# Kernel tuning notes

Hardware: AMD Instinct MI355X
Metric: run time of the kernel (lower is better)

The kernel has to match this reference:

```python
import jax, jax.numpy as jnp
import numpy as np

P, F_IN, HG, C, T, E, HOUT = 4096, 64, 64, 64, 32, 65536, 12
LEAKY_SLOPE = 0.2
LN_EPS = 1e-5


def setup_inputs() -> dict:
    key = jax.random.key(0)
    ks = jax.random.split(key, 14)
    g = lambda k, shape, scale: (jax.random.normal(k, shape, jnp.float32) * scale)
    return {
        "X": jax.random.normal(ks[0], (1, P, F_IN, T), jnp.float32),
        "edge_index": jax.random.randint(ks[1], (T, 2, E), 0, P, jnp.int32),
        # GATv2 params (single head)
        "Wl": g(ks[2], (F_IN, HG), 0.1),
        "Wr": g(ks[3], (F_IN, HG), 0.1),
        "att": g(ks[4], (HG,), 0.1),
        "gat_b": g(ks[5], (HG,), 0.02),
        # 1x1 time conv (HG -> C) and 1x1 residual conv (F_IN -> C)
        "W_time": g(ks[6], (C, HG), 0.1),
        "b_time": g(ks[7], (C,), 0.02),
        "W_res": g(ks[8], (C, F_IN), 0.1),
        "b_res": g(ks[9], (C,), 0.02),
        # LayerNorm over channel dim C
        "ln_g": jnp.ones((C,), jnp.float32),
        "ln_b": jnp.zeros((C,), jnp.float32),
        # final conv: Conv2d(in=T, out=HOUT, kernel=(1, C)) -> weight (HOUT, T, C)
        "W_final": g(ks[10], (HOUT, T, C), 0.05),
        "b_final": g(ks[11], (HOUT,), 0.02),
    }


def reference(X, edge_index, Wl, Wr, att, gat_b, W_time, b_time, W_res, b_res,
              ln_g, ln_b, W_final, b_final):
    Pn = X.shape[1]

    def gat_t(x, edges):
        # x: (P, F_IN), edges: (2, E) with edges[0]=src j, edges[1]=dst i
        src, dst = edges[0], edges[1]
        hl = x @ Wl                      # (P, HG) messages
        hr = x @ Wr                      # (P, HG) query side
        e = jax.nn.leaky_relu(hl[src] + hr[dst], LEAKY_SLOPE) @ att  # (E,)
        emax = jax.ops.segment_max(e, dst, num_segments=Pn)
        ex = jnp.exp(e - emax[dst])
        den = jax.ops.segment_sum(ex, dst, num_segments=Pn)
        alpha = ex / den[dst]            # softmax over in-edges of each dst
        return jax.ops.segment_sum(alpha[:, None] * hl[src], dst,
                                   num_segments=Pn) + gat_b  # (P, HG)

    xs = jnp.moveaxis(X[0], -1, 0)                     # (T, P, F_IN)
    X_hat = jax.nn.relu(jax.vmap(gat_t)(xs, edge_index))  # (T, P, HG)

    th = jnp.einsum('tph,ch->tpc', X_hat, W_time) + b_time  # time conv 1x1
    rs = jnp.einsum('tpf,cf->tpc', xs, W_res) + b_res       # residual conv 1x1
    y = jax.nn.relu(th + rs)                                 # (T, P, C)

    mu = jnp.mean(y, axis=-1, keepdims=True)
    var = jnp.var(y, axis=-1, keepdims=True)
    yn = (y - mu) * jax.lax.rsqrt(var + LN_EPS) * ln_g + ln_b  # (T, P, C)

    # final conv: in-channels = T, kernel (1, C) -> contract over t and c
    out = jnp.einsum('tpc,otc->po', yn, W_final) + b_final     # (P, HOUT)
    return out[None]                                           # (1, P, HOUT)
```

## Files before the change

### kernel.cpp

```cpp
#include <hip/hip_runtime.h>
#include <math.h>

#define NP 4096
#define F_IN 64
#define HG 64
#define NC 64
#define NT 32
#define NE 65536
#define HOUT 12
#define LEAKY 0.2f
#define LN_EPS 1e-5f
#define CAPC 32

template <int CTRL>
__device__ __forceinline__ float dppadd(float v, float x) {
    int r = __builtin_amdgcn_update_dpp(0, __builtin_bit_cast(int, x), CTRL, 0xF, 0xF, false);
    return v + __builtin_bit_cast(float, r);
}
__device__ __forceinline__ float rowsum16(float v) {
    v = dppadd<0x128>(v, v);
    v = dppadd<0x124>(v, v);
    v = dppadd<0x122>(v, v);
    v = dppadd<0x121>(v, v);
    return v;
}
__device__ __forceinline__ float laneXorSum(float v) {
    v += __shfl_xor(v, 16, 64);
    v += __shfl_xor(v, 32, 64);
    return v;
}

#define FMA4(Acomp, B, r)                                                     \
    acc[r][0] += (Acomp) * (B).x; acc[r][1] += (Acomp) * (B).y;               \
    acc[r][2] += (Acomp) * (B).z; acc[r][3] += (Acomp) * (B).w;

__global__ __launch_bounds__(256) void k_front(const float* __restrict__ X,
        const float* __restrict__ Wl, const float* __restrict__ Wr,
        const float* __restrict__ W_res, const float* __restrict__ b_res,
        const float* __restrict__ W_time, const float* __restrict__ bf,
        const int* __restrict__ EI,
        float* __restrict__ hl, float* __restrict__ hr, float* __restrict__ rs,
        float* __restrict__ wtT, float* __restrict__ out,
        int* __restrict__ cnt, unsigned short* __restrict__ scap) {
    __shared__ float smem[8960];
    int b = blockIdx.x;
    int tid = threadIdx.x;
    if (b < 512) {
        unsigned short (*buck)[CAPC] = (unsigned short (*)[CAPC])smem;
        int* cnts = (int*)(smem + 8192);
        int t = (b & 7) + 8 * ((b >> 3) & 3);
        int rem = b >> 5;
        int c = rem & 1, r = rem >> 1;
        cnts[tid] = 0; cnts[tid + 256] = 0;
        __syncthreads();
        const int4* srcA = (const int4*)(EI + (size_t)t * 2 * NE) + c * (NE / 8);
        const int4* dstA = (const int4*)(EI + (size_t)t * 2 * NE + NE) + c * (NE / 8);
        for (int i = tid; i < NE / 8; i += 256) {
            int4 s = srcA[i];
            int4 d = dstA[i];
            if ((d.x >> 9) == r) { int lo = d.x & 511; int sl = atomicAdd(&cnts[lo], 1); if (sl < CAPC) buck[lo][sl] = (unsigned short)s.x; }
            if ((d.y >> 9) == r) { int lo = d.y & 511; int sl = atomicAdd(&cnts[lo], 1); if (sl < CAPC) buck[lo][sl] = (unsigned short)s.y; }
            if ((d.z >> 9) == r) { int lo = d.z & 511; int sl = atomicAdd(&cnts[lo], 1); if (sl < CAPC) buck[lo][sl] = (unsigned short)s.z; }
            if ((d.w >> 9) == r) { int lo = d.w & 511; int sl = atomicAdd(&cnts[lo], 1); if (sl < CAPC) buck[lo][sl] = (unsigned short)s.w; }
        }
        __syncthreads();
        int obase = ((t * 2 + c) << 12) + (r << 9);
        cnt[obase + tid] = cnts[tid];
        cnt[obase + tid + 256] = cnts[tid + 256];
        unsigned int* dstw = (unsigned int*)(scap + (size_t)obase * CAPC);
        const unsigned int* srcw = (const unsigned int*)buck;
        for (int i = tid; i < 512 * CAPC / 2; i += 256)
            dstw[i] = srcw[i];
    } else if (b < 2560) {
        float (*xs)[F_IN][36] = (float (*)[F_IN][36])smem;
        float (*bk)[68] = (float (*)[68])(smem + 4608);
        int p0 = (b - 512) * 2;
        const float4* Xp = (const float4*)(X + (size_t)p0 * F_IN * NT);
        for (int i4 = tid; i4 < 1024; i4 += 256) {
            int pp = i4 >> 9, f = (i4 >> 3) & 63, t0 = (i4 & 7) * 4;
            *(float4*)&xs[pp][f][t0] = Xp[i4];
        }
        int ng = tid & 15, pp = (tid >> 4) & 1, tg = tid >> 5;
        int n0 = ng * 4, t0 = tg * 4;
        {
            const float4* B4 = (const float4*)Wl;
            for (int i4 = tid; i4 < 1024; i4 += 256)
                *(float4*)&bk[i4 >> 4][(i4 & 15) * 4] = B4[i4];
            __syncthreads();
            float acc[4][4];
#pragma unroll
            for (int i = 0; i < 4; ++i)
#pragma unroll
                for (int j2 = 0; j2 < 4; ++j2) acc[i][j2] = 0.f;
#pragma unroll 8
            for (int f = 0; f < F_IN; ++f) {
                float4 B = *(const float4*)&bk[f][n0];
                float4 A = *(const float4*)&xs[pp][f][t0];
                FMA4(A.x, B, 0) FMA4(A.y, B, 1) FMA4(A.z, B, 2) FMA4(A.w, B, 3)
            }
#pragma unroll
            for (int i = 0; i < 4; ++i) {
                float4 v;
                v.x = acc[i][0]; v.y = acc[i][1]; v.z = acc[i][2]; v.w = acc[i][3];
                *(float4*)&hl[((size_t)(t0 + i) * NP + p0 + pp) * HG + n0] = v;
            }
            __syncthreads();
        }
        {
            const float4* B4 = (const float4*)Wr;
            for (int i4 = tid; i4 < 1024; i4 += 256)
                *(float4*)&bk[i4 >> 4][(i4 & 15) * 4] = B4[i4];
            __syncthreads();
            float acc[4][4];
#pragma unroll
            for (int i = 0; i < 4; ++i)
#pragma unroll
                for (int j2 = 0; j2 < 4; ++j2) acc[i][j2] = 0.f;
#pragma unroll 8
            for (int f = 0; f < F_IN; ++f) {
                float4 B = *(const float4*)&bk[f][n0];
                float4 A = *(const float4*)&xs[pp][f][t0];
                FMA4(A.x, B, 0) FMA4(A.y, B, 1) FMA4(A.z, B, 2) FMA4(A.w, B, 3)
            }
#pragma unroll
            for (int i = 0; i < 4; ++i) {
                float4 v;
                v.x = acc[i][0]; v.y = acc[i][1]; v.z = acc[i][2]; v.w = acc[i][3];
                *(float4*)&hr[((size_t)(t0 + i) * NP + p0 + pp) * HG + n0] = v;
            }
            __syncthreads();
        }
        {
            for (int i = tid; i < F_IN * NC; i += 256) {
                int c = i >> 6, f = i & 63;
                bk[f][c] = W_res[i];
            }
            __syncthreads();
            float4 br4 = *(const float4*)&b_res[n0];
            float acc[4][4];
#pragma unroll
            for (int i = 0; i < 4; ++i) {
                acc[i][0] = br4.x; acc[i][1] = br4.y; acc[i][2] = br4.z; acc[i][3] = br4.w;
            }
#pragma unroll 8
            for (int f = 0; f < F_IN; ++f) {
                float4 B = *(const float4*)&bk[f][n0];
                float4 A = *(const float4*)&xs[pp][f][t0];
                FMA4(A.x, B, 0) FMA4(A.y, B, 1) FMA4(A.z, B, 2) FMA4(A.w, B, 3)
            }
#pragma unroll
            for (int i = 0; i < 4; ++i) {
                float4 v;
                v.x = acc[i][0]; v.y = acc[i][1]; v.z = acc[i][2]; v.w = acc[i][3];
                *(float4*)&rs[((size_t)(t0 + i) * NP + p0 + pp) * NC + n0] = v;
            }
        }
    } else if (b < 2576) {
        int i = (b - 2560) * 256 + tid;
        wtT[i] = W_time[(i & 63) * 64 + (i >> 6)];
    } else {
        int i = (b - 2576) * 256 + tid;
        out[i] = bf[i % HOUT];
    }
}

__global__ __launch_bounds__(256) void k_gat(const float* __restrict__ hl,
        float* __restrict__ hr,
        const int* __restrict__ cnt, const unsigned short* __restrict__ scap,
        const float* __restrict__ att, const float* __restrict__ gat_b) {
    __shared__ int sidx[4][64];
    int b = blockIdx.x;
    int k = b >> 3;
    int t = (b & 7) + 8 * (k >> 10);
    int ws = threadIdx.x >> 6;
    int i = (k & 1023) * 4 + ws;
    int lane = threadIdx.x & 63;
    int row = lane >> 4;
    int c0 = (lane & 15) * 4;
    size_t nbase = ((size_t)t * NP + i) * HG;
    const float* hlt = hl + (size_t)t * NP * HG;
    float4 r4 = *(const float4*)&hr[nbase + c0];
    float4 at4 = *(const float4*)&att[c0];
    int d0 = cnt[((t * 2 + 0) << 12) + i]; d0 = (d0 < CAPC) ? d0 : CAPC;
    int d1 = cnt[((t * 2 + 1) << 12) + i]; d1 = (d1 < CAPC) ? d1 : CAPC;
    int deg = d0 + d1;
    deg = (deg < 64) ? deg : 64;
    const unsigned short* s0 = scap + ((size_t)(((t * 2 + 0) << 12) + i)) * CAPC;
    const unsigned short* s1 = scap + ((size_t)(((t * 2 + 1) << 12) + i)) * CAPC;
    int li = (lane < deg) ? lane : 0;
    int f1 = (li >= d0);
    int idx = f1 ? (li - d0) : li;
    sidx[ws][lane] = (int)(f1 ? s1 : s0)[idx];
    float l = 0.f;
    float4 acc = {0.f, 0.f, 0.f, 0.f};
    int nfull = deg & ~7;
    int j = 0;
    for (; j < nfull; j += 8) {
        int src0 = sidx[ws][j + row];
        int src1 = sidx[ws][j + 4 + row];
        float4 h0 = *(const float4*)&hlt[((size_t)src0 << 6) + c0];
        float4 h1 = *(const float4*)&hlt[((size_t)src1 << 6) + c0];
        float4 z0, z1;
        z0.x = h0.x + r4.x; z0.y = h0.y + r4.y; z0.z = h0.z + r4.z; z0.w = h0.w + r4.w;
        z1.x = h1.x + r4.x; z1.y = h1.y + r4.y; z1.z = h1.z + r4.z; z1.w = h1.w + r4.w;
        z0.x = fmaxf(z0.x, LEAKY * z0.x); z0.y = fmaxf(z0.y, LEAKY * z0.y);
        z0.z = fmaxf(z0.z, LEAKY * z0.z); z0.w = fmaxf(z0.w, LEAKY * z0.w);
        z1.x = fmaxf(z1.x, LEAKY * z1.x); z1.y = fmaxf(z1.y, LEAKY * z1.y);
        z1.z = fmaxf(z1.z, LEAKY * z1.z); z1.w = fmaxf(z1.w, LEAKY * z1.w);
        float e0 = rowsum16(z0.x * at4.x + z0.y * at4.y + z0.z * at4.z + z0.w * at4.w);
        float e1 = rowsum16(z1.x * at4.x + z1.y * at4.y + z1.z * at4.z + z1.w * at4.w);
        float w0 = __expf(e0);
        float w1 = __expf(e1);
        l += w0 + w1;
        acc.x += w0 * h0.x + w1 * h1.x;
        acc.y += w0 * h0.y + w1 * h1.y;
        acc.z += w0 * h0.z + w1 * h1.z;
        acc.w += w0 * h0.w + w1 * h1.w;
    }
    for (; j < deg; j += 4) {
        int jj = j + row;
        int src = sidx[ws][(jj < deg) ? jj : 0];
        float4 ha = *(const float4*)&hlt[((size_t)src << 6) + c0];
        float4 za;
        za.x = ha.x + r4.x; za.y = ha.y + r4.y; za.z = ha.z + r4.z; za.w = ha.w + r4.w;
        za.x = fmaxf(za.x, LEAKY * za.x);
        za.y = fmaxf(za.y, LEAKY * za.y);
        za.z = fmaxf(za.z, LEAKY * za.z);
        za.w = fmaxf(za.w, LEAKY * za.w);
        float ep = za.x * at4.x + za.y * at4.y + za.z * at4.z + za.w * at4.w;
        float e = rowsum16(ep);
        float w = __expf(e);
        w = (jj < deg) ? w : 0.f;
        l += w;
        acc.x += w * ha.x; acc.y += w * ha.y; acc.z += w * ha.z; acc.w += w * ha.w;
    }
    float lt = laneXorSum(l);
    acc.x = laneXorSum(acc.x);
    acc.y = laneXorSum(acc.y);
    acc.z = laneXorSum(acc.z);
    acc.w = laneXorSum(acc.w);
    if (row == 0) {
        float inv = (deg > 0) ? (1.0f / lt) : 0.f;
        float4 gb = *(const float4*)&gat_b[c0];
        float4 o;
        o.x = fmaxf(acc.x * inv + gb.x, 0.f);
        o.y = fmaxf(acc.y * inv + gb.y, 0.f);
        o.z = fmaxf(acc.z * inv + gb.z, 0.f);
        o.w = fmaxf(acc.w * inv + gb.w, 0.f);
        *(float4*)&hr[nbase + c0] = o;
    }
}

__global__ __launch_bounds__(256) void k_pf(const float* __restrict__ Xhat,
        const float* __restrict__ wtT, const float* __restrict__ b_time,
        const float* __restrict__ rs, const float* __restrict__ ln_g,
        const float* __restrict__ ln_b, const float* __restrict__ Wf,
        float* __restrict__ out) {
    __shared__ float in_t[64][68];
    __shared__ float bk[64][68];
    int bx = blockIdx.x;
    int tc = bx & 15;
    int p0 = (bx >> 4) * 64;
    int tid = threadIdx.x;
    const float4* wsrc = (const float4*)wtT;
    for (int i4 = tid; i4 < 1024; i4 += 256) {
        int h = i4 >> 4, c4 = (i4 & 15) * 4;
        *(float4*)&bk[h][c4] = wsrc[i4];
    }
    int cg = tid & 15, pg = tid >> 4;
    int c0 = cg * 4, pl = pg * 4;
    float4 bt4 = *(const float4*)&b_time[c0];
    float4 lg = *(const float4*)&ln_g[c0];
    float4 lb = *(const float4*)&ln_b[c0];
    float ot[4][HOUT];
#pragma unroll
    for (int i = 0; i < 4; ++i)
#pragma unroll
        for (int o = 0; o < HOUT; ++o) ot[i][o] = 0.f;
    for (int ti = 0; ti < 2; ++ti) {
        int t = tc + ti * 16;
        __syncthreads();
        const float4* src = (const float4*)(Xhat + ((size_t)t * NP + p0) * HG);
        for (int i4 = tid; i4 < 1024; i4 += 256) {
            int pp = i4 >> 4, c4 = (i4 & 15) * 4;
            *(float4*)&in_t[pp][c4] = src[i4];
        }
        __syncthreads();
        float acc[4][4];
#pragma unroll
        for (int i = 0; i < 4; ++i) {
            acc[i][0] = bt4.x; acc[i][1] = bt4.y; acc[i][2] = bt4.z; acc[i][3] = bt4.w;
        }
#pragma unroll
        for (int k4 = 0; k4 < 16; ++k4) {
            float4 A0 = *(const float4*)&in_t[pl + 0][k4 * 4];
            float4 A1 = *(const float4*)&in_t[pl + 1][k4 * 4];
            float4 A2 = *(const float4*)&in_t[pl + 2][k4 * 4];
            float4 A3 = *(const float4*)&in_t[pl + 3][k4 * 4];
            float4 B0 = *(const float4*)&bk[k4 * 4 + 0][c0];
            FMA4(A0.x, B0, 0) FMA4(A1.x, B0, 1) FMA4(A2.x, B0, 2) FMA4(A3.x, B0, 3)
            float4 B1 = *(const float4*)&bk[k4 * 4 + 1][c0];
            FMA4(A0.y, B1, 0) FMA4(A1.y, B1, 1) FMA4(A2.y, B1, 2) FMA4(A3.y, B1, 3)
            float4 B2 = *(const float4*)&bk[k4 * 4 + 2][c0];
            FMA4(A0.z, B2, 0) FMA4(A1.z, B2, 1) FMA4(A2.z, B2, 2) FMA4(A3.z, B2, 3)
            float4 B3 = *(const float4*)&bk[k4 * 4 + 3][c0];
            FMA4(A0.w, B3, 0) FMA4(A1.w, B3, 1) FMA4(A2.w, B3, 2) FMA4(A3.w, B3, 3)
        }
        float4 ynv[4];
#pragma unroll
        for (int i = 0; i < 4; ++i) {
            size_t prow = (size_t)t * NP + p0 + pl + i;
            float4 r4 = *(const float4*)&rs[prow * NC + c0];
            float y0 = fmaxf(acc[i][0] + r4.x, 0.f), y1 = fmaxf(acc[i][1] + r4.y, 0.f);
            float y2 = fmaxf(acc[i][2] + r4.z, 0.f), y3 = fmaxf(acc[i][3] + r4.w, 0.f);
            float s = rowsum16(y0 + y1 + y2 + y3);
            float ss = rowsum16(y0 * y0 + y1 * y1 + y2 * y2 + y3 * y3);
            float mu = s * (1.f / 64.f);
            float var = ss * (1.f / 64.f) - mu * mu;
            float rsd = rsqrtf(var + LN_EPS);
            ynv[i].x = (y0 - mu) * rsd * lg.x + lb.x;
            ynv[i].y = (y1 - mu) * rsd * lg.y + lb.y;
            ynv[i].z = (y2 - mu) * rsd * lg.z + lb.z;
            ynv[i].w = (y3 - mu) * rsd * lg.w + lb.w;
        }
#pragma unroll
        for (int o = 0; o < HOUT; ++o) {
            float4 w4 = *(const float4*)&Wf[(size_t)o * NT * NC + t * NC + c0];
#pragma unroll
            for (int i = 0; i < 4; ++i)
                ot[i][o] += ynv[i].x * w4.x + ynv[i].y * w4.y
                          + ynv[i].z * w4.z + ynv[i].w * w4.w;
        }
    }
#pragma unroll
    for (int i = 0; i < 4; ++i)
#pragma unroll
        for (int o = 0; o < HOUT; ++o) ot[i][o] = rowsum16(ot[i][o]);
    if (cg == 0) {
#pragma unroll
        for (int i = 0; i < 4; ++i) {
            int p = p0 + pl + i;
#pragma unroll
            for (int o = 0; o < HOUT; ++o)
                atomicAdd(&out[p * HOUT + o], ot[i][o]);
        }
    }
}

extern "C" void kernel_launch(void* const* d_in, const int* in_sizes, int n_in,
                              void* d_out, int out_size, void* d_ws, size_t ws_size,
                              hipStream_t stream) {
    const float* X      = (const float*)d_in[0];
    const int*   EI     = (const int*)d_in[1];
    const float* Wl     = (const float*)d_in[2];
    const float* Wr     = (const float*)d_in[3];
    const float* att    = (const float*)d_in[4];
    const float* gat_b  = (const float*)d_in[5];
    const float* W_time = (const float*)d_in[6];
    const float* b_time = (const float*)d_in[7];
    const float* W_res  = (const float*)d_in[8];
    const float* b_res  = (const float*)d_in[9];
    const float* ln_g   = (const float*)d_in[10];
    const float* ln_b   = (const float*)d_in[11];
    const float* Wf     = (const float*)d_in[12];
    const float* bf     = (const float*)d_in[13];
    float* out = (float*)d_out;

    char* ws = (char*)d_ws;
    const size_t MB = 1024 * 1024;
    float* hl   = (float*)(ws);
    float* hr   = (float*)(ws + 32 * MB);
    float* rs   = (float*)(ws + 64 * MB);
    float* wtT  = (float*)(ws + 96 * MB);
    int*   cnt  = (int*)  (ws + 97 * MB);
    unsigned short* scap = (unsigned short*)(ws + 98 * MB);

    k_front<<<2768, 256, 0, stream>>>(X, Wl, Wr, W_res, b_res, W_time, bf, EI,
                                      hl, hr, rs, wtT, out, cnt, scap);
    k_gat  <<<(NT * NP) / 4, 256, 0, stream>>>(hl, hr, cnt, scap, att, gat_b);
    k_pf   <<<1024, 256, 0, stream>>>(hr, wtT, b_time, rs, ln_g, ln_b, Wf, out);
}
```

Baseline: 285.3 us.

## Fuse time conv, LayerNorm and final conv into GAT kernel with deterministic reduce

The GAT aggregation kernel now also performs the 1x1 time conv, residual add, LayerNorm and the per-timestep slice of the final conv. Each wave processes 8 nodes in a loop and keeps the W_time slice in registers. Per-timestep partial outputs go to a workspace buffer, and a small new kernel sums them over T and adds the bias, replacing the atomicAdd path and the out-initialisation blocks. This removes the X_hat write/read round trip and the separate k_pf GEMM. In exchange it adds register pressure (wreg[16]), serial per-node work per wave, and a third launch.

```diff
diff --git a/kernel.cpp b/kernel.cpp
--- a/kernel.cpp
+++ b/kernel.cpp
@@ -37,10 +37,10 @@
 __global__ __launch_bounds__(256) void k_front(const float* __restrict__ X,
         const float* __restrict__ Wl, const float* __restrict__ Wr,
         const float* __restrict__ W_res, const float* __restrict__ b_res,
-        const float* __restrict__ W_time, const float* __restrict__ bf,
+        const float* __restrict__ W_time,
         const int* __restrict__ EI,
         float* __restrict__ hl, float* __restrict__ hr, float* __restrict__ rs,
-        float* __restrict__ wtT, float* __restrict__ out,
+        float* __restrict__ wtT,
         int* __restrict__ cnt, unsigned short* __restrict__ scap) {
     __shared__ float smem[8960];
     int b = blockIdx.x;
@@ -155,196 +155,154 @@
                 *(float4*)&rs[((size_t)(t0 + i) * NP + p0 + pp) * NC + n0] = v;
             }
         }
-    } else if (b < 2576) {
+    } else {
         int i = (b - 2560) * 256 + tid;
         wtT[i] = W_time[(i & 63) * 64 + (i >> 6)];
-    } else {
-        int i = (b - 2576) * 256 + tid;
-        out[i] = bf[i % HOUT];
     }
 }
 
 __global__ __launch_bounds__(256) void k_gat(const float* __restrict__ hl,
-        float* __restrict__ hr,
+        const float* __restrict__ hr, const float* __restrict__ rs,
         const int* __restrict__ cnt, const unsigned short* __restrict__ scap,
-        const float* __restrict__ att, const float* __restrict__ gat_b) {
+        const float* __restrict__ att, const float* __restrict__ gat_b,
+        const float* __restrict__ wtT, const float* __restrict__ b_time,
+        const float* __restrict__ ln_g, const float* __restrict__ ln_b,
+        const float* __restrict__ Wf, float* __restrict__ pout) {
     __shared__ int sidx[4][64];
+    __shared__ float xbuf[4][64];
     int b = blockIdx.x;
-    int k = b >> 3;
-    int t = (b & 7) + 8 * (k >> 10);
+    int t = (b & 7) + 8 * (b >> 10);
+    int pc = (b >> 3) & 127;
     int ws = threadIdx.x >> 6;
-    int i = (k & 1023) * 4 + ws;
     int lane = threadIdx.x & 63;
     int row = lane >> 4;
-    int c0 = (lane & 15) * 4;
-    size_t nbase = ((size_t)t * NP + i) * HG;
+    int cg = lane & 15;
+    int c0 = cg * 4;
     const float* hlt = hl + (size_t)t * NP * HG;
-    float4 r4 = *(const float4*)&hr[nbase + c0];
     float4 at4 = *(const float4*)&att[c0];
-    int d0 = cnt[((t * 2 + 0) << 12) + i]; d0 = (d0 < CAPC) ? d0 : CAPC;
-    int d1 = cnt[((t * 2 + 1) << 12) + i]; d1 = (d1 < CAPC) ? d1 : CAPC;
-    int deg = d0 + d1;
-    deg = (deg < 64) ? deg : 64;
-    const unsigned short* s0 = scap + ((size_t)(((t * 2 + 0) << 12) + i)) * CAPC;
-    const unsigned short* s1 = scap + ((size_t)(((t * 2 + 1) << 12) + i)) * CAPC;
-    int li = (lane < deg) ? lane : 0;
-    int f1 = (li >= d0);
-    int idx = f1 ? (li - d0) : li;
-    sidx[ws][lane] = (int)(f1 ? s1 : s0)[idx];
-    float l = 0.f;
-    float4 acc = {0.f, 0.f, 0.f, 0.f};
-    int nfull = deg & ~7;
-    int j = 0;
-    for (; j < nfull; j += 8) {
-        int src0 = sidx[ws][j + row];
-        int src1 = sidx[ws][j + 4 + row];
-        float4 h0 = *(const float4*)&hlt[((size_t)src0 << 6) + c0];
-        float4 h1 = *(const float4*)&hlt[((size_t)src1 << 6) + c0];
-        float4 z0, z1;
-        z0.x = h0.x + r4.x; z0.y = h0.y + r4.y; z0.z = h0.z + r4.z; z0.w = h0.w + r4.w;
-        z1.x = h1.x + r4.x; z1.y = h1.y + r4.y; z1.z = h1.z + r4.z; z1.w = h1.w + r4.w;
-        z0.x = fmaxf(z0.x, LEAKY * z0.x); z0.y = fmaxf(z0.y, LEAKY * z0.y);
-        z0.z = fmaxf(z0.z, LEAKY * z0.z); z0.w = fmaxf(z0.w, LEAKY * z0.w);
-        z1.x = fmaxf(z1.x, LEAKY * z1.x); z1.y = fmaxf(z1.y, LEAKY * z1.y);
-        z1.z = fmaxf(z1.z, LEAKY * z1.z); z1.w = fmaxf(z1.w, LEAKY * z1.w);
-        float e0 = rowsum16(z0.x * at4.x + z0.y * at4.y + z0.z * at4.z + z0.w * at4.w);
-        float e1 = rowsum16(z1.x * at4.x + z1.y * at4.y + z1.z * at4.z + z1.w * at4.w);
-        float w0 = __expf(e0);
-        float w1 = __expf(e1);
-        l += w0 + w1;
-        acc.x += w0 * h0.x + w1 * h1.x;
-        acc.y += w0 * h0.y + w1 * h1.y;
-        acc.z += w0 * h0.z + w1 * h1.z;
-        acc.w += w0 * h0.w + w1 * h1.w;
+    float4 gb4 = *(const float4*)&gat_b[c0];
+    float4 bt4 = *(const float4*)&b_time[c0];
+    float4 lg  = *(const float4*)&ln_g[c0];
+    float4 lb  = *(const float4*)&ln_b[c0];
+    float4 wreg[16];
+    {
+        const float4* wq = (const float4*)wtT + (size_t)(row * 16) * (HG / 4) + cg;
+#pragma unroll
+        for (int i = 0; i < 16; ++i) wreg[i] = wq[i * (HG / 4)];
     }
-    for (; j < deg; j += 4) {
-        int jj = j + row;
-        int src = sidx[ws][(jj < deg) ? jj : 0];
-        float4 ha = *(const float4*)&hlt[((size_t)src << 6) + c0];
-        float4 za;
-        za.x = ha.x + r4.x; za.y = ha.y + r4.y; za.z = ha.z + r4.z; za.w = ha.w + r4.w;
-        za.x = fmaxf(za.x, LEAKY * za.x);
-        za.y = fmaxf(za.y, LEAKY * za.y);
-        za.z = fmaxf(za.z, LEAKY * za.z);
-        za.w = fmaxf(za.w, LEAKY * za.w);
-        float ep = za.x * at4.x + za.y * at4.y + za.z * at4.z + za.w * at4.w;
-        float e = rowsum16(ep);
-        float w = __expf(e);
-        w = (jj < deg) ? w : 0.f;
-        l += w;
-        acc.x += w * ha.x; acc.y += w * ha.y; acc.z += w * ha.z; acc.w += w * ha.w;
+    float4 wf0 = *(const float4*)&Wf[((size_t)(3 * row + 0) * NT + t) * NC + c0];
+    float4 wf1 = *(const float4*)&Wf[((size_t)(3 * row + 1) * NT + t) * NC + c0];
+    float4 wf2 = *(const float4*)&Wf[((size_t)(3 * row + 2) * NT + t) * NC + c0];
+
+    for (int q = 0; q < 8; ++q) {
+        int p = pc * 32 + ws * 8 + q;
+        size_t nbase = ((size_t)t * NP + p) * HG;
+        float4 r4 = *(const float4*)&hr[nbase + c0];
+        int d0 = cnt[((t * 2 + 0) << 12) + p]; d0 = (d0 < CAPC) ? d0 : CAPC;
+        int d1 = cnt[((t * 2 + 1) << 12) + p]; d1 = (d1 < CAPC) ? d1 : CAPC;
+        int deg = d0 + d1;
+        const unsigned short* s0 = scap + ((size_t)(((t * 2 + 0) << 12) + p)) * CAPC;
+        const unsigned short* s1 = scap + ((size_t)(((t * 2 + 1) << 12) + p)) * CAPC;
+        int li = (lane < deg) ? lane : 0;
+        int f1 = (li >= d0);
+        int idx = f1 ? (li - d0) : li;
+        sidx[ws][lane] = (int)(f1 ? s1 : s0)[idx];
+        float l = 0.f;
+        float4 acc = {0.f, 0.f, 0.f, 0.f};
+        int nfull = deg & ~7;
+        int j = 0;
+        for (; j < nfull; j += 8) {
+            int src0 = sidx[ws][j + row];
+            int src1 = sidx[ws][j + 4 + row];
+            float4 h0 = *(const float4*)&hlt[((size_t)src0 << 6) + c0];
+            float4 h1 = *(const float4*)&hlt[((size_t)src1 << 6) + c0];
+            float4 z0, z1;
+            z0.x = h0.x + r4.x; z0.y = h0.y + r4.y; z0.z = h0.z + r4.z; z0.w = h0.w + r4.w;
+            z1.x = h1.x + r4.x; z1.y = h1.y + r4.y; z1.z = h1.z + r4.z; z1.w = h1.w + r4.w;
+            z0.x = fmaxf(z0.x, LEAKY * z0.x); z0.y = fmaxf(z0.y, LEAKY * z0.y);
+            z0.z = fmaxf(z0.z, LEAKY * z0.z); z0.w = fmaxf(z0.w, LEAKY * z0.w);
+            z1.x = fmaxf(z1.x, LEAKY * z1.x); z1.y = fmaxf(z1.y, LEAKY * z1.y);
+            z1.z = fmaxf(z1.z, LEAKY * z1.z); z1.w = fmaxf(z1.w, LEAKY * z1.w);
+            float e0 = rowsum16(z0.x * at4.x + z0.y * at4.y + z0.z * at4.z + z0.w * at4.w);
+            float e1 = rowsum16(z1.x * at4.x + z1.y * at4.y + z1.z * at4.z + z1.w * at4.w);
+            float w0 = __expf(e0);
+            float w1 = __expf(e1);
+            l += w0 + w1;
+            acc.x += w0 * h0.x + w1 * h1.x;
+            acc.y += w0 * h0.y + w1 * h1.y;
+            acc.z += w0 * h0.z + w1 * h1.z;
+            acc.w += w0 * h0.w + w1 * h1.w;
+        }
+        for (; j < deg; j += 4) {
+            int jj = j + row;
+            int src = sidx[ws][(jj < deg) ? jj : 0];
+            float4 ha = *(const float4*)&hlt[((size_t)src << 6) + c0];
+            float4 za;
+            za.x = ha.x + r4.x; za.y = ha.y + r4.y; za.z = ha.z + r4.z; za.w = ha.w + r4.w;
+            za.x = fmaxf(za.x, LEAKY * za.x);
+            za.y = fmaxf(za.y, LEAKY * za.y);
+            za.z = fmaxf(za.z, LEAKY * za.z);
+            za.w = fmaxf(za.w, LEAKY * za.w);
+            float ep = za.x * at4.x + za.y * at4.y + za.z * at4.z + za.w * at4.w;
+            float e = rowsum16(ep);
+            float w = __expf(e);
+            w = (jj < deg) ? w : 0.f;
+            l += w;
+            acc.x += w * ha.x; acc.y += w * ha.y; acc.z += w * ha.z; acc.w += w * ha.w;
+        }
+        float lt = laneXorSum(l);
+        acc.x = laneXorSum(acc.x);
+        acc.y = laneXorSum(acc.y);
+        acc.z = laneXorSum(acc.z);
+        acc.w = laneXorSum(acc.w);
+        float inv = (deg > 0) ? (1.0f / lt) : 0.f;
+        float4 xh;
+        xh.x = fmaxf(acc.x * inv + gb4.x, 0.f);
+        xh.y = fmaxf(acc.y * inv + gb4.y, 0.f);
+        xh.z = fmaxf(acc.z * inv + gb4.z, 0.f);
+        xh.w = fmaxf(acc.w * inv + gb4.w, 0.f);
+        if (row == 0) *(float4*)&xbuf[ws][c0] = xh;
+        float4 y4 = {0.f, 0.f, 0.f, 0.f};
+#pragma unroll
+        for (int i = 0; i < 16; ++i) {
+            float xf = xbuf[ws][row * 16 + i];
+            y4.x += xf * wreg[i].x; y4.y += xf * wreg[i].y;
+            y4.z += xf * wreg[i].z; y4.w += xf * wreg[i].w;
+        }
+        y4.x = laneXorSum(y4.x); y4.y = laneXorSum(y4.y);
+        y4.z = laneXorSum(y4.z); y4.w = laneXorSum(y4.w);
+        float4 rs4 = *(const float4*)&rs[((size_t)t * NP + p) * NC + c0];
+        float y0 = fmaxf(y4.x + bt4.x + rs4.x, 0.f);
+        float y1 = fmaxf(y4.y + bt4.y + rs4.y, 0.f);
+        float y2 = fmaxf(y4.z + bt4.z + rs4.z, 0.f);
+        float y3 = fmaxf(y4.w + bt4.w + rs4.w, 0.f);
+        float s  = rowsum16(y0 + y1 + y2 + y3);
+        float ss = rowsum16(y0 * y0 + y1 * y1 + y2 * y2 + y3 * y3);
+        float mu = s * (1.f / 64.f);
+        float var = ss * (1.f / 64.f) - mu * mu;
+        float rsd = rsqrtf(var + LN_EPS);
+        float n0 = (y0 - mu) * rsd * lg.x + lb.x;
+        float n1 = (y1 - mu) * rsd * lg.y + lb.y;
+        float n2 = (y2 - mu) * rsd * lg.z + lb.z;
+        float n3 = (y3 - mu) * rsd * lg.w + lb.w;
+        float o0 = n0 * wf0.x + n1 * wf0.y + n2 * wf0.z + n3 * wf0.w;
+        float o1 = n0 * wf1.x + n1 * wf1.y + n2 * wf1.z + n3 * wf1.w;
+        float o2 = n0 * wf2.x + n1 * wf2.y + n2 * wf2.z + n3 * wf2.w;
+        o0 = rowsum16(o0); o1 = rowsum16(o1); o2 = rowsum16(o2);
+        if (cg == 0) {
+            float* pp = pout + ((size_t)t * NP + p) * HOUT + 3 * row;
+            pp[0] = o0; pp[1] = o1; pp[2] = o2;
+        }
     }
-    float lt = laneXorSum(l);
-    acc.x = laneXorSum(acc.x);
-    acc.y = laneXorSum(acc.y);
-    acc.z = laneXorSum(acc.z);
-    acc.w = laneXorSum(acc.w);
-    if (row == 0) {
-        float inv = (deg > 0) ? (1.0f / lt) : 0.f;
-        float4 gb = *(const float4*)&gat_b[c0];
-        float4 o;
-        o.x = fmaxf(acc.x * inv + gb.x, 0.f);
-        o.y = fmaxf(acc.y * inv + gb.y, 0.f);
-        o.z = fmaxf(acc.z * inv + gb.z, 0.f);
-        o.w = fmaxf(acc.w * inv + gb.w, 0.f);
-        *(float4*)&hr[nbase + c0] = o;
-    }
-}
-
-__global__ __launch_bounds__(256) void k_pf(const float* __restrict__ Xhat,
-        const float* __restrict__ wtT, const float* __restrict__ b_time,
-        const float* __restrict__ rs, const float* __restrict__ ln_g,
-        const float* __restrict__ ln_b, const float* __restrict__ Wf,
-        float* __restrict__ out) {
-    __shared__ float in_t[64][68];
-    __shared__ float bk[64][68];
-    int bx = blockIdx.x;
-    int tc = bx & 15;
-    int p0 = (bx >> 4) * 64;
-    int tid = threadIdx.x;
-    const float4* wsrc = (const float4*)wtT;
-    for (int i4 = tid; i4 < 1024; i4 += 256) {
-        int h = i4 >> 4, c4 = (i4 & 15) * 4;
-        *(float4*)&bk[h][c4] = wsrc[i4];
-    }
-    int cg = tid & 15, pg = tid >> 4;
-    int c0 = cg * 4, pl = pg * 4;
-    float4 bt4 = *(const float4*)&b_time[c0];
-    float4 lg = *(const float4*)&ln_g[c0];
-    float4 lb = *(const float4*)&ln_b[c0];
-    float ot[4][HOUT];
-#pragma unroll
-    for (int i = 0; i < 4; ++i)
-#pragma unroll
-        for (int o = 0; o < HOUT; ++o) ot[i][o] = 0.f;
-    for (int ti = 0; ti < 2; ++ti) {
-        int t = tc + ti * 16;
-        __syncthreads();
-        const float4* src = (const float4*)(Xhat + ((size_t)t * NP + p0) * HG);
-        for (int i4 = tid; i4 < 1024; i4 += 256) {
-            int pp = i4 >> 4, c4 = (i4 & 15) * 4;
-            *(float4*)&in_t[pp][c4] = src[i4];
-        }
-        __syncthreads();
-        float acc[4][4];
-#pragma unroll
-        for (int i = 0; i < 4; ++i) {
-            acc[i][0] = bt4.x; acc[i][1] = bt4.y; acc[i][2] = bt4.z; acc[i][3] = bt4.w;
-        }
-#pragma unroll
-        for (int k4 = 0; k4 < 16; ++k4) {
-            float4 A0 = *(const float4*)&in_t[pl + 0][k4 * 4];
-            float4 A1 = *(const float4*)&in_t[pl + 1][k4 * 4];
-            float4 A2 = *(const float4*)&in_t[pl + 2][k4 * 4];
-            float4 A3 = *(const float4*)&in_t[pl + 3][k4 * 4];
-            float4 B0 = *(const float4*)&bk[k4 * 4 + 0][c0];
-            FMA4(A0.x, B0, 0) FMA4(A1.x, B0, 1) FMA4(A2.x, B0, 2) FMA4(A3.x, B0, 3)
-            float4 B1 = *(const float4*)&bk[k4 * 4 + 1][c0];
-            FMA4(A0.y, B1, 0) FMA4(A1.y, B1, 1) FMA4(A2.y, B1, 2) FMA4(A3.y, B1, 3)
-            float4 B2 = *(const float4*)&bk[k4 * 4 + 2][c0];
-            FMA4(A0.z, B2, 0) FMA4(A1.z, B2, 1) FMA4(A2.z, B2, 2) FMA4(A3.z, B2, 3)
-            float4 B3 = *(const float4*)&bk[k4 * 4 + 3][c0];
-            FMA4(A0.w, B3, 0) FMA4(A1.w, B3, 1) FMA4(A2.w, B3, 2) FMA4(A3.w, B3, 3)
-        }
-        float4 ynv[4];
-#pragma unroll
-        for (int i = 0; i < 4; ++i) {
-            size_t prow = (size_t)t * NP + p0 + pl + i;
-            float4 r4 = *(const float4*)&rs[prow * NC + c0];
-            float y0 = fmaxf(acc[i][0] + r4.x, 0.f), y1 = fmaxf(acc[i][1] + r4.y, 0.f);
-            float y2 = fmaxf(acc[i][2] + r4.z, 0.f), y3 = fmaxf(acc[i][3] + r4.w, 0.f);
-            float s = rowsum16(y0 + y1 + y2 + y3);
-            float ss = rowsum16(y0 * y0 + y1 * y1 + y2 * y2 + y3 * y3);
-            float mu = s * (1.f / 64.f);
-            float var = ss * (1.f / 64.f) - mu * mu;
-            float rsd = rsqrtf(var + LN_EPS);
-            ynv[i].x = (y0 - mu) * rsd * lg.x + lb.x;
-            ynv[i].y = (y1 - mu) * rsd * lg.y + lb.y;
-            ynv[i].z = (y2 - mu) * rsd * lg.z + lb.z;
-            ynv[i].w = (y3 - mu) * rsd * lg.w + lb.w;
-        }
-#pragma unroll
-        for (int o = 0; o < HOUT; ++o) {
-            float4 w4 = *(const float4*)&Wf[(size_t)o * NT * NC + t * NC + c0];
-#pragma unroll
-            for (int i = 0; i < 4; ++i)
-                ot[i][o] += ynv[i].x * w4.x + ynv[i].y * w4.y
-                          + ynv[i].z * w4.z + ynv[i].w * w4.w;
-        }
-    }
-#pragma unroll
-    for (int i = 0; i < 4; ++i)
-#pragma unroll
-        for (int o = 0; o < HOUT; ++o) ot[i][o] = rowsum16(ot[i][o]);
-    if (cg == 0) {
-#pragma unroll
-        for (int i = 0; i < 4; ++i) {
-            int p = p0 + pl + i;
-#pragma unroll
-            for (int o = 0; o < HOUT; ++o)
-                atomicAdd(&out[p * HOUT + o], ot[i][o]);
-        }
-    }
+}
+
+__global__ __launch_bounds__(256) void k_out(const float* __restrict__ pout,
+        const float* __restrict__ bf, float* __restrict__ out) {
+    int k = blockIdx.x * 256 + threadIdx.x;
+    float s = bf[k % HOUT];
+#pragma unroll 8
+    for (int t = 0; t < NT; ++t) s += pout[(size_t)t * (NP * HOUT) + k];
+    out[k] = s;
 }
 
 extern "C" void kernel_launch(void* const* d_in, const int* in_sizes, int n_in,
@@ -374,9 +332,11 @@
     float* wtT  = (float*)(ws + 96 * MB);
     int*   cnt  = (int*)  (ws + 97 * MB);
     unsigned short* scap = (unsigned short*)(ws + 98 * MB);
-
-    k_front<<<2768, 256, 0, stream>>>(X, Wl, Wr, W_res, b_res, W_time, bf, EI,
-                                      hl, hr, rs, wtT, out, cnt, scap);
-    k_gat  <<<(NT * NP) / 4, 256, 0, stream>>>(hl, hr, cnt, scap, att, gat_b);
-    k_pf   <<<1024, 256, 0, stream>>>(hr, wtT, b_time, rs, ln_g, ln_b, Wf, out);
-}
+    float* pout = (float*)(ws + 114 * MB);
+
+    k_front<<<2576, 256, 0, stream>>>(X, Wl, Wr, W_res, b_res, W_time, EI,
+                                      hl, hr, rs, wtT, cnt, scap);
+    k_gat  <<<4096, 256, 0, stream>>>(hl, hr, rs, cnt, scap, att, gat_b,
+                                      wtT, b_time, ln_g, ln_b, Wf, pout);
+    k_out  <<<NP * HOUT / 256, 256, 0, stream>>>(pout, bf, out);
+}
```

New measurement: 285.0 us. About the same (-0.1%).
